# Performance work log

Measured on AMD Instinct MI355X. Metric: run time of the kernel, lower is better.

Reference implementation:

```python
import jax, jax.numpy as jnp
import numpy as np

VOCAB, D, A, H, F = 100000, 128, 128, 4, 128  # embed dim == attention_dim (residual), 4 heads, final_dim
B, L, L2 = 64, 200, 50
NEG = float(-2**32 + 1)


def setup_inputs() -> dict:
    key = jax.random.key(0)
    ks = jax.random.split(key, 12)
    queries = jax.random.randint(ks[0], (B, L), 0, VOCAB)
    keys = jax.random.randint(ks[1], (B, L, L2), 0, VOCAB)
    E = jax.random.normal(ks[2], (VOCAB, D), dtype=jnp.float32) * 0.02
    Wq = jax.random.normal(ks[3], (D, A), dtype=jnp.float32) * (1.0 / np.sqrt(D))
    bq = jnp.zeros((A,), jnp.float32)
    Wk = jax.random.normal(ks[4], (D, A), dtype=jnp.float32) * (1.0 / np.sqrt(D))
    bk = jnp.zeros((A,), jnp.float32)
    Wv = jax.random.normal(ks[5], (D, A), dtype=jnp.float32) * (1.0 / np.sqrt(D))
    bv = jnp.zeros((A,), jnp.float32)
    Wf = jax.random.normal(ks[6], (A, F), dtype=jnp.float32) * (1.0 / np.sqrt(A))
    bf = jnp.zeros((F,), jnp.float32)
    return {"queries": queries, "keys": keys, "E": E, "Wq": Wq, "bq": bq,
            "Wk": Wk, "bk": bk, "Wv": Wv, "bv": bv, "Wf": Wf, "bf": bf}


def reference(queries, keys, E, Wq, bq, Wk, bk, Wv, bv, Wf, bf):
    q_emb = E[queries]                      # [B, L, D]
    k_emb = E[keys]                         # [B, L, L2, D]
    Q = q_emb @ Wq + bq                     # [B, L, A]
    K = k_emb @ Wk + bk                     # [B, L, L2, A]
    V = k_emb @ Wv + bv                     # [B, L, L2, A]
    d = A // H
    Qh = Q.reshape(Q.shape[0], Q.shape[1], H, d)                       # [B, L, H, d]
    Kh = K.reshape(K.shape[0], K.shape[1], K.shape[2], H, d)           # [B, L, L2, H, d]
    Vh = V.reshape(V.shape[0], V.shape[1], V.shape[2], H, d)
    # per-(b,l) query attends over its L2 keys, per head; scale by sqrt(depth)
    scores = jnp.einsum('blhd,blkhd->bhlk', Qh, Kh) / jnp.sqrt(jnp.asarray(d, Q.dtype))
    # padding mask from embedded-key content: sign(|sum_d k_emb|) == 0 -> masked
    key_mask = jnp.sign(jnp.abs(jnp.sum(k_emb, axis=-1)))              # [B, L, L2]
    scores = jnp.where(key_mask[:, None, :, :] == 0, NEG, scores)
    attn = jax.nn.softmax(scores, axis=-1)                             # [B, H, L, L2]
    out = jnp.einsum('bhlk,blkhd->blhd', attn, Vh)
    out = out.reshape(out.shape[0], out.shape[1], A)                   # [B, L, A]
    out = out + q_emb                                                  # residual
    return out @ Wf + bf                                               # [B, L, F]
```

## Files before the change

### kernel.cpp

```cpp
#include <hip/hip_runtime.h>
#include <stdint.h>

#define DN 128
#define AN 128
#define HN 4
#define FN 128
#define L2N 50
#define NPOS (64*200)
#define NEGC (-4294967295.0f)

#define OFF_MTWB 0
#define OFF_GTB  40960
#define OFF_CB   73728
#define OFF_U    74368
#define OFF_R    3351168
#define OFF_PV   4989568

typedef __fp16 half2v __attribute__((ext_vector_type(2)));
typedef __fp16 f16x8  __attribute__((ext_vector_type(8)));
typedef float  f32x4  __attribute__((ext_vector_type(4)));
union frg { uint4 u; f16x8 h; };

__device__ __forceinline__ float dot2(uint32_t a, uint32_t b, float c) {
#if __has_builtin(__builtin_amdgcn_fdot2)
    union { uint32_t u; half2v h; } ca, cb; ca.u = a; cb.u = b;
    return __builtin_amdgcn_fdot2(ca.h, cb.h, c, false);
#else
    union { uint32_t u; _Float16 h[2]; } ca, cb; ca.u = a; cb.u = b;
    return c + (float)ca.h[0]*(float)cb.h[0] + (float)ca.h[1]*(float)cb.h[1];
#endif
}
__device__ __forceinline__ uint32_t packh2(float x, float y) {
    union { _Float16 h[2]; uint32_t u; } c; c.h[0] = (_Float16)x; c.h[1] = (_Float16)y;
    return c.u;
}
__device__ __forceinline__ float lo16f(uint32_t u) {
    union { uint32_t u; _Float16 h[2]; } c; c.u = u; return (float)c.h[0];
}
__device__ __forceinline__ float hi16f(uint32_t u) {
    union { uint32_t u; _Float16 h[2]; } c; c.u = u; return (float)c.h[1];
}

__global__ __launch_bounds__(256) void k0_pre(
    const float* __restrict__ Wq, const float* __restrict__ bq,
    const float* __restrict__ Wk, const float* __restrict__ bk,
    const float* __restrict__ Wv, const float* __restrict__ bv,
    const float* __restrict__ Wf, const float* __restrict__ bfb,
    float* __restrict__ ws)
{
    uint32_t* MTWB = (uint32_t*)ws + OFF_MTWB;
    uint32_t* GTBw = (uint32_t*)ws + OFF_GTB;
    float*    CB   = ws + OFF_CB;
    const int idx = blockIdx.x*256 + threadIdx.x;

    if (idx < 40960) {
        int jj = idx & 3, lane = (idx>>2)&63, kk = (idx>>8)&3, tn = idx>>10;
        int outc = tn*16 + (lane&15);
        int dd2  = kk*16 + (lane>>4)*4 + jj;
        int dd0  = 2*dd2, dd1 = dd0+1;
        float s0, s1;
        if (outc < 512) {
            int h = outc >> 7, d = outc & 127;
            const float* wk = Wk + d*AN + h*32;
            const float* q0 = Wq + dd0*AN + h*32;
            const float* q1 = Wq + dd1*AN + h*32;
            s0 = 0.f; s1 = 0.f;
            #pragma unroll 8
            for (int j = 0; j < 32; ++j) { float w = wk[j]; s0 += q0[j]*w; s1 += q1[j]*w; }
        } else {
            int f = outc - 512;
            s0 = Wf[dd0*FN + f]; s1 = Wf[dd1*FN + f];
        }
        MTWB[idx] = packh2(s0, s1);
    } else if (idx < 73728) {
        int i2 = idx - 40960;
        int jj = i2 & 3, lane = (i2>>2)&63, kk = (i2>>8)&15, tn = i2>>12;
        int f  = tn*16 + (lane&15);
        int j2 = kk*16 + (lane>>4)*4 + jj;
        int hd0 = 2*j2;
        int h = hd0 >> 7, d0 = hd0 & 127, d1 = d0+1;
        const float* v0 = Wv + d0*AN + h*32;
        const float* v1 = Wv + d1*AN + h*32;
        float s0 = 0.f, s1 = 0.f;
        #pragma unroll 8
        for (int a = 0; a < 32; ++a) {
            float wf = Wf[(h*32+a)*FN + f];
            s0 += v0[a]*wf; s1 += v1[a]*wf;
        }
        GTBw[i2] = packh2(s0, s1);
    } else {
        int c = idx - 73728;
        if (c < 512) {
            int h = c >> 7, d = c & 127;
            float s = 0.f;
            #pragma unroll 8
            for (int j = 0; j < 32; ++j) s += Wk[d*AN + h*32 + j]*bq[h*32 + j];
            CB[c] = s;
        } else if (c < 640) {
            int f = c - 512;
            float s = bfb[f];
            for (int a = 0; a < AN; ++a) s += bv[a]*Wf[a*FN + f];
            CB[c] = s;
        }
    }
}

__global__ __launch_bounds__(256) void k1_proj(
    const int* __restrict__ queries, const float* __restrict__ E,
    float* __restrict__ ws)
{
    const uint32_t* MTWB = (const uint32_t*)ws + OFF_MTWB;
    const float*    CB   = ws + OFF_CB;
    uint32_t* U = (uint32_t*)ws + OFF_U;
    float*    R = ws + OFF_R;

    const int t = threadIdx.x, wv = t >> 6, ln = t & 63;
    const int W  = blockIdx.x*4 + wv;
    const int tm = W / 5, g = W - tm*5;
    const int m = ln & 15, q = ln >> 4;
    const int pos0 = tm*16 + q*4;

    const int qidx = queries[tm*16 + m];
    const float* Eq = E + (size_t)qidx * DN;

    frg a[4];
    #pragma unroll
    for (int kk = 0; kk < 4; ++kk) {
        float4 e0 = *(const float4*)(Eq + kk*32 + q*8);
        float4 e1 = *(const float4*)(Eq + kk*32 + q*8 + 4);
        a[kk].u.x = packh2(e0.x, e0.y);
        a[kk].u.y = packh2(e0.z, e0.w);
        a[kk].u.z = packh2(e1.x, e1.y);
        a[kk].u.w = packh2(e1.z, e1.w);
    }

    #pragma unroll 1
    for (int i = 0; i < 8; ++i) {
        const int tn = g*8 + i;
        const float cb = CB[tn*16 + m];
        f32x4 c = {cb, cb, cb, cb};
        #pragma unroll
        for (int kk = 0; kk < 4; ++kk) {
            frg b; b.u = *(const uint4*)(MTWB + ((size_t)(tn*4 + kk)*64 + ln)*4);
            c = __builtin_amdgcn_mfma_f32_16x16x32_f16(a[kk].h, b.h, c, 0, 0, 0);
        }
        if (tn < 32) {
            float p0 = __shfl_xor(c[0], 1);
            float p1 = __shfl_xor(c[1], 1);
            float p2 = __shfl_xor(c[2], 1);
            float p3 = __shfl_xor(c[3], 1);
            if ((ln & 1) == 0) {
                const int ucol = tn*8 + (m >> 1);
                U[(size_t)(pos0+0)*256 + ucol] = packh2(c[0], p0);
                U[(size_t)(pos0+1)*256 + ucol] = packh2(c[1], p1);
                U[(size_t)(pos0+2)*256 + ucol] = packh2(c[2], p2);
                U[(size_t)(pos0+3)*256 + ucol] = packh2(c[3], p3);
            }
        } else {
            const int f = (tn - 32)*16 + m;
            R[(size_t)(pos0+0)*128 + f] = c[0];
            R[(size_t)(pos0+1)*128 + f] = c[1];
            R[(size_t)(pos0+2)*128 + f] = c[2];
            R[(size_t)(pos0+3)*128 + f] = c[3];
        }
    }
}

__global__ __launch_bounds__(128) void k2_attn(
    const int* __restrict__ keys, const float* __restrict__ E,
    float* __restrict__ ws)
{
    __shared__ __align__(16) uint32_t kT[2][64][51];
    __shared__ __align__(16) uint32_t U_s[2][256];
    __shared__ __align__(8)  uint32_t attnT[2][L2N][2];

    const uint32_t* U  = (const uint32_t*)ws + OFF_U;
    uint32_t*       PV = (uint32_t*)ws + OFF_PV;

    const int t = threadIdx.x, wv = t >> 6, ln = t & 63;
    const int pos0 = blockIdx.x * 2;

    ((uint4*)&U_s[0][0])[t] = ((const uint4*)(U + (size_t)pos0*256))[t];

    const int* kptr = keys + (size_t)(pos0 + wv)*L2N;
    uint32_t kreg[L2N];
    {
        float2 f0 = *(const float2*)(E + (size_t)kptr[0]*DN + 2*ln);
        float2 f1 = *(const float2*)(E + (size_t)kptr[1]*DN + 2*ln);
        float2 f2 = *(const float2*)(E + (size_t)kptr[2]*DN + 2*ln);
        float2 f3 = *(const float2*)(E + (size_t)kptr[3]*DN + 2*ln);
        #pragma unroll
        for (int r = 0; r < L2N; ++r) {
            float2 cur;
            if ((r&3)==0) cur=f0; else if ((r&3)==1) cur=f1; else if ((r&3)==2) cur=f2; else cur=f3;
            if (r+4 < L2N) {
                float2 nx = *(const float2*)(E + (size_t)kptr[r+4]*DN + 2*ln);
                if ((r&3)==0) f0=nx; else if ((r&3)==1) f1=nx; else if ((r&3)==2) f2=nx; else f3=nx;
            }
            uint32_t u = packh2(cur.x, cur.y);
            kreg[r] = u;
            kT[wv][ln][r] = u;
        }
    }
    __syncthreads();

    {
        const int r  = ln;
        const int rc = (r < L2N) ? r : 0;
        float acc0=0.f, acc1=0.f, acc2=0.f, acc3=0.f, ksum=0.f;
        const uint32_t ONE2 = 0x3C003C00u;
        #pragma unroll 4
        for (int dp = 0; dp < 64; dp += 4) {
            uint4 u0 = *(const uint4*)&U_s[wv][0*64 + dp];
            uint4 u1 = *(const uint4*)&U_s[wv][1*64 + dp];
            uint4 u2 = *(const uint4*)&U_s[wv][2*64 + dp];
            uint4 u3 = *(const uint4*)&U_s[wv][3*64 + dp];
            uint32_t k0 = kT[wv][dp+0][rc];
            uint32_t k1 = kT[wv][dp+1][rc];
            uint32_t k2 = kT[wv][dp+2][rc];
            uint32_t k3 = kT[wv][dp+3][rc];
            acc0 = dot2(k0,u0.x,acc0); acc0 = dot2(k1,u0.y,acc0);
            acc0 = dot2(k2,u0.z,acc0); acc0 = dot2(k3,u0.w,acc0);
            acc1 = dot2(k0,u1.x,acc1); acc1 = dot2(k1,u1.y,acc1);
            acc1 = dot2(k2,u1.z,acc1); acc1 = dot2(k3,u1.w,acc1);
            acc2 = dot2(k0,u2.x,acc2); acc2 = dot2(k1,u2.y,acc2);
            acc2 = dot2(k2,u2.z,acc2); acc2 = dot2(k3,u2.w,acc2);
            acc3 = dot2(k0,u3.x,acc3); acc3 = dot2(k1,u3.y,acc3);
            acc3 = dot2(k2,u3.z,acc3); acc3 = dot2(k3,u3.w,acc3);
            ksum = dot2(k0,ONE2,ksum); ksum = dot2(k1,ONE2,ksum);
            ksum = dot2(k2,ONE2,ksum); ksum = dot2(k3,ONE2,ksum);
        }
        float sc[4];
        sc[0] = acc0 * 0.17677669529663687f;
        sc[1] = acc1 * 0.17677669529663687f;
        sc[2] = acc2 * 0.17677669529663687f;
        sc[3] = acc3 * 0.17677669529663687f;
        if (ksum == 0.0f) { sc[0]=NEGC; sc[1]=NEGC; sc[2]=NEGC; sc[3]=NEGC; }
        if (r >= L2N) { sc[0]=-__builtin_inff(); sc[1]=-__builtin_inff();
                        sc[2]=-__builtin_inff(); sc[3]=-__builtin_inff(); }
        float w[4];
        #pragma unroll
        for (int h = 0; h < 4; ++h) {
            float m = sc[h];
            m = fmaxf(m, __shfl_xor(m,32)); m = fmaxf(m, __shfl_xor(m,16));
            m = fmaxf(m, __shfl_xor(m, 8)); m = fmaxf(m, __shfl_xor(m, 4));
            m = fmaxf(m, __shfl_xor(m, 2)); m = fmaxf(m, __shfl_xor(m, 1));
            float e = (r < L2N) ? __expf(sc[h] - m) : 0.f;
            float s = e;
            s += __shfl_xor(s,32); s += __shfl_xor(s,16); s += __shfl_xor(s,8);
            s += __shfl_xor(s, 4); s += __shfl_xor(s, 2); s += __shfl_xor(s,1);
            w[h] = e / s;
        }
        if (r < L2N) {
            attnT[wv][r][0] = packh2(w[0], w[1]);
            attnT[wv][r][1] = packh2(w[2], w[3]);
        }
    }
    __syncthreads();

    {
        float pa0=0.f,pb0=0.f,pa1=0.f,pb1=0.f,pa2=0.f,pb2=0.f,pa3=0.f,pb3=0.f;
        #pragma unroll
        for (int r = 0; r < L2N; ++r) {
            uint2 aw = *(const uint2*)&attnT[wv][r][0];
            float w0 = lo16f(aw.x), w1 = hi16f(aw.x);
            float w2 = lo16f(aw.y), w3 = hi16f(aw.y);
            uint32_t kp = kreg[r];
            float kx = lo16f(kp), ky = hi16f(kp);
            pa0 += w0*kx; pb0 += w0*ky;
            pa1 += w1*kx; pb1 += w1*ky;
            pa2 += w2*kx; pb2 += w2*ky;
            pa3 += w3*kx; pb3 += w3*ky;
        }
        uint32_t* PVp = PV + (size_t)(pos0 + wv)*256;
        PVp[0*64 + ln] = packh2(pa0, pb0);
        PVp[1*64 + ln] = packh2(pa1, pb1);
        PVp[2*64 + ln] = packh2(pa2, pb2);
        PVp[3*64 + ln] = packh2(pa3, pb3);
    }
}

__global__ __launch_bounds__(256) void k3_out(
    const float* __restrict__ ws, float* __restrict__ out)
{
    const uint32_t* GTB = (const uint32_t*)ws + OFF_GTB;
    const uint32_t* PV  = (const uint32_t*)ws + OFF_PV;
    const float*    R   = ws + OFF_R;

    const int t = threadIdx.x, wv = t >> 6, ln = t & 63;
    const int W  = blockIdx.x*4 + wv;
    const int tm = W >> 2, g = W & 3;
    const int m = ln & 15, q = ln >> 4;
    const int pos0 = tm*16 + q*4;

    frg a[16];
    const uint32_t* PVa = PV + (size_t)(tm*16 + m)*256;
    #pragma unroll
    for (int kk = 0; kk < 16; ++kk)
        a[kk].u = *(const uint4*)(PVa + kk*16 + q*4);

    #pragma unroll 1
    for (int i = 0; i < 2; ++i) {
        const int nt = g*2 + i;
        const int f = nt*16 + m;
        f32x4 c;
        c[0] = R[(size_t)(pos0+0)*128 + f];
        c[1] = R[(size_t)(pos0+1)*128 + f];
        c[2] = R[(size_t)(pos0+2)*128 + f];
        c[3] = R[(size_t)(pos0+3)*128 + f];
        #pragma unroll
        for (int kk = 0; kk < 16; ++kk) {
            frg b; b.u = *(const uint4*)(GTB + ((size_t)(nt*16 + kk)*64 + ln)*4);
            c = __builtin_amdgcn_mfma_f32_16x16x32_f16(a[kk].h, b.h, c, 0, 0, 0);
        }
        out[(size_t)(pos0+0)*128 + f] = c[0];
        out[(size_t)(pos0+1)*128 + f] = c[1];
        out[(size_t)(pos0+2)*128 + f] = c[2];
        out[(size_t)(pos0+3)*128 + f] = c[3];
    }
}

extern "C" void kernel_launch(void* const* d_in, const int* in_sizes, int n_in,
                              void* d_out, int out_size, void* d_ws, size_t ws_size,
                              hipStream_t stream) {
    const int* queries = (const int*)d_in[0];
    const int* keys    = (const int*)d_in[1];
    const float* E   = (const float*)d_in[2];
    const float* Wq  = (const float*)d_in[3];
    const float* bq  = (const float*)d_in[4];
    const float* Wk  = (const float*)d_in[5];
    const float* bk  = (const float*)d_in[6];
    const float* Wv  = (const float*)d_in[7];
    const float* bv  = (const float*)d_in[8];
    const float* Wf  = (const float*)d_in[9];
    const float* bfb = (const float*)d_in[10];
    float* ws = (float*)d_ws;
    float* o  = (float*)d_out;

    hipLaunchKernelGGL(k0_pre,  dim3(291),  dim3(256), 0, stream,
                       Wq, bq, Wk, bk, Wv, bv, Wf, bfb, ws);
    hipLaunchKernelGGL(k1_proj, dim3(1000), dim3(256), 0, stream, queries, E, ws);
    hipLaunchKernelGGL(k2_attn, dim3(6400), dim3(128), 0, stream, keys, E, ws);
    hipLaunchKernelGGL(k3_out,  dim3(800),  dim3(256), 0, stream, ws, o);
}
```

Measured before the change: 185.8 us.

## Use MFMA for attention scores and packed dot2 for PV in k2_attn

The attention kernel now computes per-head scores, and the key-sum used for the padding mask, with 16x16x32 f16 MFMA instructions, replacing the per-lane dot2 loops. A ones column in the B operand yields the mask sum. Softmax works on MFMA fragments with fewer cross-lane shuffles and no second block barrier. The PV accumulation uses fdot2 on key pairs packed in registers. The weight-precompute kernel is also restructured to stage weights in shared memory with fewer blocks. The cost is MFMA work wasted on padded rows and columns, plus more registers.

```diff
diff --git a/kernel.cpp b/kernel.cpp
--- a/kernel.cpp
+++ b/kernel.cpp
@@ -33,12 +33,6 @@
 __device__ __forceinline__ uint32_t packh2(float x, float y) {
     union { _Float16 h[2]; uint32_t u; } c; c.h[0] = (_Float16)x; c.h[1] = (_Float16)y;
     return c.u;
-}
-__device__ __forceinline__ float lo16f(uint32_t u) {
-    union { uint32_t u; _Float16 h[2]; } c; c.u = u; return (float)c.h[0];
-}
-__device__ __forceinline__ float hi16f(uint32_t u) {
-    union { uint32_t u; _Float16 h[2]; } c; c.u = u; return (float)c.h[1];
 }
 
 __global__ __launch_bounds__(256) void k0_pre(
@@ -51,56 +45,81 @@
     uint32_t* MTWB = (uint32_t*)ws + OFF_MTWB;
     uint32_t* GTBw = (uint32_t*)ws + OFF_GTB;
     float*    CB   = ws + OFF_CB;
-    const int idx = blockIdx.x*256 + threadIdx.x;
-
-    if (idx < 40960) {
-        int jj = idx & 3, lane = (idx>>2)&63, kk = (idx>>8)&3, tn = idx>>10;
-        int outc = tn*16 + (lane&15);
-        int dd2  = kk*16 + (lane>>4)*4 + jj;
-        int dd0  = 2*dd2, dd1 = dd0+1;
-        float s0, s1;
-        if (outc < 512) {
-            int h = outc >> 7, d = outc & 127;
-            const float* wk = Wk + d*AN + h*32;
-            const float* q0 = Wq + dd0*AN + h*32;
-            const float* q1 = Wq + dd1*AN + h*32;
-            s0 = 0.f; s1 = 0.f;
-            #pragma unroll 8
-            for (int j = 0; j < 32; ++j) { float w = wk[j]; s0 += q0[j]*w; s1 += q1[j]*w; }
-        } else {
-            int f = outc - 512;
-            s0 = Wf[dd0*FN + f]; s1 = Wf[dd1*FN + f];
-        }
-        MTWB[idx] = packh2(s0, s1);
-    } else if (idx < 73728) {
-        int i2 = idx - 40960;
-        int jj = i2 & 3, lane = (i2>>2)&63, kk = (i2>>8)&15, tn = i2>>12;
-        int f  = tn*16 + (lane&15);
-        int j2 = kk*16 + (lane>>4)*4 + jj;
-        int hd0 = 2*j2;
-        int h = hd0 >> 7, d0 = hd0 & 127, d1 = d0+1;
-        const float* v0 = Wv + d0*AN + h*32;
-        const float* v1 = Wv + d1*AN + h*32;
+    const int b = blockIdx.x, t = threadIdx.x;
+
+    if (b < 128) {
+        __shared__ float Aq[32][33];
+        __shared__ float Ak[16][33];
+        const int tn = b >> 2, kk = b & 3;
+        const int h = tn >> 3;
+        for (int i = t >> 5; i < 32; i += 8)
+            Aq[i][t & 31] = Wq[(32*kk + i)*AN + h*32 + (t & 31)];
+        for (int i = t >> 5; i < 16; i += 8)
+            Ak[i][t & 31] = Wk[((tn & 7)*16 + i)*AN + h*32 + (t & 31)];
+        __syncthreads();
+        const int lane = t >> 2, jj = t & 3;
+        const int dl0 = 8*(lane >> 4) + 2*jj;
+        const int ol  = lane & 15;
+        float s0 = 0.f, s1 = 0.f;
+        #pragma unroll 8
+        for (int j = 0; j < 32; ++j) {
+            float wkv = Ak[ol][j];
+            s0 += Aq[dl0][j]*wkv;
+            s1 += Aq[dl0+1][j]*wkv;
+        }
+        MTWB[b*256 + t] = packh2(s0, s1);
+    } else if (b < 256) {
+        __shared__ float Vv[32][33];
+        __shared__ float Wl[32][17];
+        const int g = b - 128, tn = g >> 4, kk = g & 15;
+        const int h = kk >> 2;
+        for (int i = t >> 5; i < 32; i += 8)
+            Vv[i][t & 31] = Wv[(32*(kk & 3) + i)*AN + h*32 + (t & 31)];
+        for (int i = t; i < 512; i += 256) {
+            int a0 = i >> 4, fl = i & 15;
+            Wl[a0][fl] = Wf[(h*32 + a0)*FN + tn*16 + fl];
+        }
+        __syncthreads();
+        const int lane = t >> 2, jj = t & 3;
+        const int dl0 = 8*(lane >> 4) + 2*jj;
+        const int fl  = lane & 15;
         float s0 = 0.f, s1 = 0.f;
         #pragma unroll 8
         for (int a = 0; a < 32; ++a) {
-            float wf = Wf[(h*32+a)*FN + f];
-            s0 += v0[a]*wf; s1 += v1[a]*wf;
-        }
-        GTBw[i2] = packh2(s0, s1);
+            float wfv = Wl[a][fl];
+            s0 += Vv[dl0][a]*wfv;
+            s1 += Vv[dl0+1][a]*wfv;
+        }
+        GTBw[g*256 + t] = packh2(s0, s1);
+    } else if (b == 256) {
+        const int f = t & 127;
+        const int d0 = (t >> 7)*32;
+        for (int dd2 = d0; dd2 < d0 + 32; ++dd2) {
+            uint32_t v = packh2(Wf[(2*dd2)*FN + f], Wf[(2*dd2+1)*FN + f]);
+            int tn = 32 + (f >> 4);
+            int lane = ((dd2 >> 2) & 3)*16 + (f & 15);
+            MTWB[tn*1024 + (dd2 >> 4)*256 + lane*4 + (dd2 & 3)] = v;
+        }
     } else {
-        int c = idx - 73728;
-        if (c < 512) {
+        __shared__ float WkL[128][129];
+        for (int i4 = t; i4 < 4096; i4 += 256) {
+            float4 v = *(const float4*)(Wk + i4*4);
+            int d = (i4*4) >> 7, col = (i4*4) & 127;
+            WkL[d][col]   = v.x; WkL[d][col+1] = v.y;
+            WkL[d][col+2] = v.z; WkL[d][col+3] = v.w;
+        }
+        __syncthreads();
+        for (int c = t; c < 512; c += 256) {
             int h = c >> 7, d = c & 127;
             float s = 0.f;
             #pragma unroll 8
-            for (int j = 0; j < 32; ++j) s += Wk[d*AN + h*32 + j]*bq[h*32 + j];
+            for (int j = 0; j < 32; ++j) s += WkL[d][h*32 + j]*bq[h*32 + j];
             CB[c] = s;
-        } else if (c < 640) {
-            int f = c - 512;
-            float s = bfb[f];
-            for (int a = 0; a < AN; ++a) s += bv[a]*Wf[a*FN + f];
-            CB[c] = s;
+        }
+        if (t < 128) {
+            float s = bfb[t];
+            for (int a = 0; a < AN; ++a) s += bv[a]*Wf[a*FN + t];
+            CB[512 + t] = s;
         }
     }
 }
@@ -170,113 +189,130 @@
     const int* __restrict__ keys, const float* __restrict__ E,
     float* __restrict__ ws)
 {
-    __shared__ __align__(16) uint32_t kT[2][64][51];
-    __shared__ __align__(16) uint32_t U_s[2][256];
-    __shared__ __align__(8)  uint32_t attnT[2][L2N][2];
+    __shared__ uint32_t kT[2][64][51];
+    __shared__ __align__(16) uint32_t attnP[2][32][4];
 
     const uint32_t* U  = (const uint32_t*)ws + OFF_U;
     uint32_t*       PV = (uint32_t*)ws + OFF_PV;
 
     const int t = threadIdx.x, wv = t >> 6, ln = t & 63;
-    const int pos0 = blockIdx.x * 2;
-
-    ((uint4*)&U_s[0][0])[t] = ((const uint4*)(U + (size_t)pos0*256))[t];
-
-    const int* kptr = keys + (size_t)(pos0 + wv)*L2N;
-    uint32_t kreg[L2N];
+    const int pos = blockIdx.x*2 + wv;
+    const int m16 = ln & 15, q = ln >> 4;
+    const int* kp = keys + (size_t)pos * L2N;
+
+    frg bu[4];
+    #pragma unroll
+    for (int kk = 0; kk < 4; ++kk) {
+        if (m16 < 4)
+            bu[kk].u = *(const uint4*)(U + (size_t)pos*256 + m16*64 + kk*16 + q*4);
+        else if (m16 == 4)
+            bu[kk].u = make_uint4(0x3C003C00u, 0x3C003C00u, 0x3C003C00u, 0x3C003C00u);
+        else
+            bu[kk].u = make_uint4(0u, 0u, 0u, 0u);
+    }
+
+    uint32_t klo2[25], khi2[25];
     {
-        float2 f0 = *(const float2*)(E + (size_t)kptr[0]*DN + 2*ln);
-        float2 f1 = *(const float2*)(E + (size_t)kptr[1]*DN + 2*ln);
-        float2 f2 = *(const float2*)(E + (size_t)kptr[2]*DN + 2*ln);
-        float2 f3 = *(const float2*)(E + (size_t)kptr[3]*DN + 2*ln);
-        #pragma unroll
-        for (int r = 0; r < L2N; ++r) {
-            float2 cur;
-            if ((r&3)==0) cur=f0; else if ((r&3)==1) cur=f1; else if ((r&3)==2) cur=f2; else cur=f3;
-            if (r+4 < L2N) {
-                float2 nx = *(const float2*)(E + (size_t)kptr[r+4]*DN + 2*ln);
-                if ((r&3)==0) f0=nx; else if ((r&3)==1) f1=nx; else if ((r&3)==2) f2=nx; else f3=nx;
+        float2 a0 = *(const float2*)(E + (size_t)kp[0]*DN + 2*ln);
+        float2 a1 = *(const float2*)(E + (size_t)kp[1]*DN + 2*ln);
+        float2 b0 = *(const float2*)(E + (size_t)kp[2]*DN + 2*ln);
+        float2 b1 = *(const float2*)(E + (size_t)kp[3]*DN + 2*ln);
+        #pragma unroll
+        for (int r2 = 0; r2 < 25; ++r2) {
+            float2 c0 = a0, c1 = a1;
+            a0 = b0; a1 = b1;
+            if (r2 < 23) {
+                b0 = *(const float2*)(E + (size_t)kp[2*r2+4]*DN + 2*ln);
+                b1 = *(const float2*)(E + (size_t)kp[2*r2+5]*DN + 2*ln);
             }
-            uint32_t u = packh2(cur.x, cur.y);
-            kreg[r] = u;
-            kT[wv][ln][r] = u;
+            uint32_t ka = packh2(c0.x, c0.y);
+            uint32_t kb = packh2(c1.x, c1.y);
+            kT[wv][ln][2*r2]   = ka;
+            kT[wv][ln][2*r2+1] = kb;
+            klo2[r2] = (ka & 0xFFFFu) | (kb << 16);
+            khi2[r2] = (ka >> 16)     | (kb & 0xFFFF0000u);
         }
     }
     __syncthreads();
 
+    f32x4 cc[4] = {{0,0,0,0},{0,0,0,0},{0,0,0,0},{0,0,0,0}};
+    #pragma unroll
+    for (int kk = 0; kk < 4; ++kk) {
+        const int dp0 = kk*16 + q*4;
+        #pragma unroll
+        for (int tt = 0; tt < 4; ++tt) {
+            frg a;
+            const int r = tt*16 + m16;
+            a.u.x = kT[wv][dp0+0][r];
+            a.u.y = kT[wv][dp0+1][r];
+            a.u.z = kT[wv][dp0+2][r];
+            a.u.w = kT[wv][dp0+3][r];
+            cc[tt] = __builtin_amdgcn_mfma_f32_16x16x32_f16(a.h, bu[kk].h, cc[tt], 0, 0, 0);
+        }
+    }
+
+    float w[4][4];
     {
-        const int r  = ln;
-        const int rc = (r < L2N) ? r : 0;
-        float acc0=0.f, acc1=0.f, acc2=0.f, acc3=0.f, ksum=0.f;
-        const uint32_t ONE2 = 0x3C003C00u;
-        #pragma unroll 4
-        for (int dp = 0; dp < 64; dp += 4) {
-            uint4 u0 = *(const uint4*)&U_s[wv][0*64 + dp];
-            uint4 u1 = *(const uint4*)&U_s[wv][1*64 + dp];
-            uint4 u2 = *(const uint4*)&U_s[wv][2*64 + dp];
-            uint4 u3 = *(const uint4*)&U_s[wv][3*64 + dp];
-            uint32_t k0 = kT[wv][dp+0][rc];
-            uint32_t k1 = kT[wv][dp+1][rc];
-            uint32_t k2 = kT[wv][dp+2][rc];
-            uint32_t k3 = kT[wv][dp+3][rc];
-            acc0 = dot2(k0,u0.x,acc0); acc0 = dot2(k1,u0.y,acc0);
-            acc0 = dot2(k2,u0.z,acc0); acc0 = dot2(k3,u0.w,acc0);
-            acc1 = dot2(k0,u1.x,acc1); acc1 = dot2(k1,u1.y,acc1);
-            acc1 = dot2(k2,u1.z,acc1); acc1 = dot2(k3,u1.w,acc1);
-            acc2 = dot2(k0,u2.x,acc2); acc2 = dot2(k1,u2.y,acc2);
-            acc2 = dot2(k2,u2.z,acc2); acc2 = dot2(k3,u2.w,acc2);
-            acc3 = dot2(k0,u3.x,acc3); acc3 = dot2(k1,u3.y,acc3);
-            acc3 = dot2(k2,u3.z,acc3); acc3 = dot2(k3,u3.w,acc3);
-            ksum = dot2(k0,ONE2,ksum); ksum = dot2(k1,ONE2,ksum);
-            ksum = dot2(k2,ONE2,ksum); ksum = dot2(k3,ONE2,ksum);
-        }
-        float sc[4];
-        sc[0] = acc0 * 0.17677669529663687f;
-        sc[1] = acc1 * 0.17677669529663687f;
-        sc[2] = acc2 * 0.17677669529663687f;
-        sc[3] = acc3 * 0.17677669529663687f;
-        if (ksum == 0.0f) { sc[0]=NEGC; sc[1]=NEGC; sc[2]=NEGC; sc[3]=NEGC; }
-        if (r >= L2N) { sc[0]=-__builtin_inff(); sc[1]=-__builtin_inff();
-                        sc[2]=-__builtin_inff(); sc[3]=-__builtin_inff(); }
-        float w[4];
-        #pragma unroll
-        for (int h = 0; h < 4; ++h) {
-            float m = sc[h];
-            m = fmaxf(m, __shfl_xor(m,32)); m = fmaxf(m, __shfl_xor(m,16));
-            m = fmaxf(m, __shfl_xor(m, 8)); m = fmaxf(m, __shfl_xor(m, 4));
-            m = fmaxf(m, __shfl_xor(m, 2)); m = fmaxf(m, __shfl_xor(m, 1));
-            float e = (r < L2N) ? __expf(sc[h] - m) : 0.f;
-            float s = e;
-            s += __shfl_xor(s,32); s += __shfl_xor(s,16); s += __shfl_xor(s,8);
-            s += __shfl_xor(s, 4); s += __shfl_xor(s, 2); s += __shfl_xor(s,1);
-            w[h] = e / s;
-        }
-        if (r < L2N) {
-            attnT[wv][r][0] = packh2(w[0], w[1]);
-            attnT[wv][r][1] = packh2(w[2], w[3]);
-        }
-    }
-    __syncthreads();
+        float sc[4][4];
+        #pragma unroll
+        for (int tt = 0; tt < 4; ++tt)
+            #pragma unroll
+            for (int rg = 0; rg < 4; ++rg) {
+                float kv = __shfl(cc[tt][rg], (ln & 48) | 4);
+                float s  = cc[tt][rg] * 0.17677669529663687f;
+                s = (kv == 0.0f) ? NEGC : s;
+                int r = tt*16 + q*4 + rg;
+                sc[tt][rg] = (r < L2N) ? s : -__builtin_inff();
+            }
+        float mx = sc[0][0];
+        #pragma unroll
+        for (int tt = 0; tt < 4; ++tt)
+            #pragma unroll
+            for (int rg = 0; rg < 4; ++rg) mx = fmaxf(mx, sc[tt][rg]);
+        mx = fmaxf(mx, __shfl_xor(mx, 16));
+        mx = fmaxf(mx, __shfl_xor(mx, 32));
+        float sum = 0.f;
+        #pragma unroll
+        for (int tt = 0; tt < 4; ++tt)
+            #pragma unroll
+            for (int rg = 0; rg < 4; ++rg) {
+                float e = __expf(sc[tt][rg] - mx);
+                w[tt][rg] = e;
+                sum += e;
+            }
+        sum += __shfl_xor(sum, 16);
+        sum += __shfl_xor(sum, 32);
+        float inv = 1.0f / sum;
+        #pragma unroll
+        for (int tt = 0; tt < 4; ++tt)
+            #pragma unroll
+            for (int rg = 0; rg < 4; ++rg) w[tt][rg] *= inv;
+    }
+
+    if (m16 < 4) {
+        #pragma unroll
+        for (int tt = 0; tt < 4; ++tt) {
+            attnP[wv][8*tt + 2*q    ][m16] = packh2(w[tt][0], w[tt][1]);
+            attnP[wv][8*tt + 2*q + 1][m16] = packh2(w[tt][2], w[tt][3]);
+        }
+    }
 
     {
-        float pa0=0.f,pb0=0.f,pa1=0.f,pb1=0.f,pa2=0.f,pb2=0.f,pa3=0.f,pb3=0.f;
-        #pragma unroll
-        for (int r = 0; r < L2N; ++r) {
-            uint2 aw = *(const uint2*)&attnT[wv][r][0];
-            float w0 = lo16f(aw.x), w1 = hi16f(aw.x);
-            float w2 = lo16f(aw.y), w3 = hi16f(aw.y);
-            uint32_t kp = kreg[r];
-            float kx = lo16f(kp), ky = hi16f(kp);
-            pa0 += w0*kx; pb0 += w0*ky;
-            pa1 += w1*kx; pb1 += w1*ky;
-            pa2 += w2*kx; pb2 += w2*ky;
-            pa3 += w3*kx; pb3 += w3*ky;
-        }
-        uint32_t* PVp = PV + (size_t)(pos0 + wv)*256;
-        PVp[0*64 + ln] = packh2(pa0, pb0);
-        PVp[1*64 + ln] = packh2(pa1, pb1);
-        PVp[2*64 + ln] = packh2(pa2, pb2);
-        PVp[3*64 + ln] = packh2(pa3, pb3);
+        float l0=0,l1=0,l2=0,l3=0,h0=0,h1=0,h2=0,h3=0;
+        #pragma unroll
+        for (int r2 = 0; r2 < 25; ++r2) {
+            uint4 wp = *(const uint4*)&attnP[wv][r2][0];
+            uint32_t lo = klo2[r2], hi = khi2[r2];
+            l0 = dot2(lo, wp.x, l0); h0 = dot2(hi, wp.x, h0);
+            l1 = dot2(lo, wp.y, l1); h1 = dot2(hi, wp.y, h1);
+            l2 = dot2(lo, wp.z, l2); h2 = dot2(hi, wp.z, h2);
+            l3 = dot2(lo, wp.w, l3); h3 = dot2(hi, wp.w, h3);
+        }
+        uint32_t* PVp = PV + (size_t)pos*256;
+        PVp[0*64 + ln] = packh2(l0, h0);
+        PVp[1*64 + ln] = packh2(l1, h1);
+        PVp[2*64 + ln] = packh2(l2, h2);
+        PVp[3*64 + ln] = packh2(l3, h3);
     }
 }
 
@@ -337,7 +373,7 @@
     float* ws = (float*)d_ws;
     float* o  = (float*)d_out;
 
-    hipLaunchKernelGGL(k0_pre,  dim3(291),  dim3(256), 0, stream,
+    hipLaunchKernelGGL(k0_pre,  dim3(258),  dim3(256), 0, stream,
                        Wq, bq, Wk, bk, Wv, bv, Wf, bfb, ws);
     hipLaunchKernelGGL(k1_proj, dim3(1000), dim3(256), 0, stream, queries, E, ws);
     hipLaunchKernelGGL(k2_attn, dim3(6400), dim3(128), 0, stream, keys, E, ws);
```

Result: no change. 188.4 us (+1.4%).
